# Optimization experiments

Hardware: AMD Instinct MI355X
Metric: run time of the kernel (lower is better)

Reference implementation:

```python
import jax, jax.numpy as jnp
import numpy as np

B, T, E, H = 4, 4096, 1024, 64

def setup_inputs() -> dict:
    key = jax.random.key(0)
    kx, kk, kq, kv = jax.random.split(key, 4)
    x = jax.random.normal(kx, (B, T, E), dtype=jnp.float32)
    Wk = jax.random.normal(kk, (E, H), dtype=jnp.float32) * (E ** -0.5)
    Wq = jax.random.normal(kq, (E, H), dtype=jnp.float32) * (E ** -0.5)
    Wv = jax.random.normal(kv, (E, H), dtype=jnp.float32) * (E ** -0.5)
    return {"x": x, "Wk": Wk, "Wq": Wq, "Wv": Wv}

def reference(x, Wk, Wq, Wv):
    # x: [B, T, E]; single causal attention head, dropout rate 0 (no-op)
    t = x.shape[1]
    k = jnp.einsum('bte,eh->bth', x, Wk)  # [B,T,H]
    q = jnp.einsum('bte,eh->bth', x, Wq)  # [B,T,H]
    v = jnp.einsum('bte,eh->bth', x, Wv)  # [B,T,H]
    scores = jnp.einsum('bqh,bkh->bqk', q, k) * (k.shape[-1] ** -0.5)  # [B,T,T]
    causal = jnp.tril(jnp.ones((t, t), dtype=bool))
    scores = jnp.where(causal, scores, -jnp.inf)
    attn = jax.nn.softmax(scores, axis=-1)
    return jnp.einsum('bqk,bkh->bqh', attn, v)  # [B,T,H]
```

## Files before the change

kernel.cpp:

```cpp
#include <hip/hip_runtime.h>
#include <hip/hip_bf16.h>

typedef short short8 __attribute__((ext_vector_type(8)));
typedef short short4v __attribute__((ext_vector_type(4)));
typedef float float4v __attribute__((ext_vector_type(4)));
typedef float f32x4 __attribute__((ext_vector_type(4)));

#define NEG_HUGE (-1e30f)
#define QK_SCALE 0.1803368801111204f

__device__ __forceinline__ unsigned short f2bf(float f) {
  union { __hip_bfloat16 h; unsigned short u; } c;
  c.h = __float2bfloat16(f);
  return c.u;
}

#define MFMA16(a, b, c) __builtin_amdgcn_mfma_f32_16x16x32_bf16((a), (b), (c), 0, 0, 0)

__global__ __launch_bounds__(256) void wtrans_kernel(
    const float* __restrict__ Wk, const float* __restrict__ Wq,
    const float* __restrict__ Wv, unsigned short* __restrict__ Wt) {
  int mat = blockIdx.x >> 4, kb = blockIdx.x & 15;
  const float* W = (mat == 0) ? Wk : ((mat == 1) ? Wq : Wv);
  float qscale = (mat == 1) ? QK_SCALE : 1.0f;
  __shared__ float tile[64][65];
  int tid = threadIdx.x;
  int n = tid & 63, k0 = tid >> 6;
#pragma unroll
  for (int i = 0; i < 16; i++) {
    int k = i * 4 + k0;
    tile[k][n] = W[(kb * 64 + k) * 64 + n];
  }
  __syncthreads();
  int n2 = tid >> 2, c = tid & 3;
  unsigned short tmp[16];
#pragma unroll
  for (int j = 0; j < 16; j++) tmp[j] = f2bf(tile[c * 16 + j][n2] * qscale);
  unsigned short* dst = Wt + (mat * 64 + n2) * 1024 + kb * 64 + c * 16;
  *(short8*)dst = *(short8*)tmp;
  *(short8*)(dst + 8) = *(short8*)(tmp + 8);
}

__global__ __launch_bounds__(512, 2) void proj_kernel(
    const float* __restrict__ x, const unsigned short* __restrict__ Wt,
    unsigned short* __restrict__ Kb, unsigned short* __restrict__ Qb,
    unsigned short* __restrict__ Vt) {
  __shared__ unsigned short x_l[2][64 * 64];
  __shared__ unsigned short w_l[2][192 * 64];
  int tid = threadIdx.x;
  int w = tid >> 6, lane = tid & 63;
  int wm = w >> 1, wn = w & 1;
  int g = lane >> 4, r = lane & 15;
  int row0 = blockIdx.x * 64;

  int xr = tid >> 3, xc16 = tid & 7;
  const float* xp = &x[(size_t)(row0 + xr) * 1024 + xc16 * 8];
  int xelem = xr * 64 + ((xc16 * 8) ^ ((xr & 7) << 3));
  const unsigned short* wp[3];
  int welem[3];
#pragma unroll
  for (int i = 0; i < 3; i++) {
    int c = tid + i * 512;
    int wr = c >> 3, wc16 = c & 7;
    wp[i] = &Wt[(size_t)wr * 1024 + wc16 * 8];
    welem[i] = wr * 64 + ((wc16 * 8) ^ ((wr & 7) << 3));
  }
  int swz = (r & 7) << 3;

  f32x4 acc[6];
#pragma unroll
  for (int nf = 0; nf < 6; nf++) acc[nf] = (f32x4){0.f, 0.f, 0.f, 0.f};

  float4v xa = *(const float4v*)(xp);
  float4v xb = *(const float4v*)(xp + 4);
  short8 wv[3];
#pragma unroll
  for (int i = 0; i < 3; i++) wv[i] = *(const short8*)(wp[i]);

  for (int t = 0; t < 16; t++) {
    int buf = t & 1;
    {
      unsigned short t8[8];
      t8[0] = f2bf(xa[0]); t8[1] = f2bf(xa[1]); t8[2] = f2bf(xa[2]); t8[3] = f2bf(xa[3]);
      t8[4] = f2bf(xb[0]); t8[5] = f2bf(xb[1]); t8[6] = f2bf(xb[2]); t8[7] = f2bf(xb[3]);
      *(short8*)&x_l[buf][xelem] = *(short8*)t8;
#pragma unroll
      for (int i = 0; i < 3; i++) *(short8*)&w_l[buf][welem[i]] = wv[i];
    }
    if (t < 15) {
      int k0 = (t + 1) * 64;
      xa = *(const float4v*)(xp + k0);
      xb = *(const float4v*)(xp + k0 + 4);
#pragma unroll
      for (int i = 0; i < 3; i++) wv[i] = *(const short8*)(wp[i] + k0);
    }
    __syncthreads();
#pragma unroll
    for (int ks = 0; ks < 2; ks++) {
      short8 af = *(short8*)&x_l[buf][(wm * 16 + r) * 64 + ((ks * 32 + g * 8) ^ swz)];
#pragma unroll
      for (int nf = 0; nf < 6; nf++) {
        short8 bf = *(short8*)&w_l[buf][(wn * 96 + nf * 16 + r) * 64 + ((ks * 32 + g * 8) ^ swz)];
        acc[nf] = MFMA16(af, bf, acc[nf]);
      }
    }
  }
#pragma unroll
  for (int nf = 0; nf < 6; nf++) {
    int col = wn * 96 + nf * 16 + r;
    if (col < 128) {
      int mat = col >> 6, h = col & 63;
      unsigned short* dst = (mat == 0) ? Kb : Qb;
#pragma unroll
      for (int reg = 0; reg < 4; reg++) {
        int grow = row0 + wm * 16 + g * 4 + reg;
        dst[(size_t)grow * 64 + h] = f2bf(acc[nf][reg]);
      }
    } else {
      int h = col & 63;
      int grow0 = row0 + wm * 16 + g * 4;
      unsigned short t4[4];
#pragma unroll
      for (int reg = 0; reg < 4; reg++) t4[reg] = f2bf(acc[nf][reg]);
      int kv6 = grow0 & 63;
      int nfb = (kv6 >> 4) & 3, gb = (kv6 >> 2) & 3;
      int s0 = (nfb >> 1) * 32 + gb * 8 + (nfb & 1) * 4;
      size_t off = ((size_t)(grow0 >> 12) * 64 + h) * 4096 +
                   ((size_t)(grow0 & 4095) & ~(size_t)63) + s0;
      *(short4v*)&Vt[off] = *(short4v*)t4;
    }
  }
}

__global__ __launch_bounds__(256, 3) void attn_kernel(
    const unsigned short* __restrict__ Kb, const unsigned short* __restrict__ Qb,
    const unsigned short* __restrict__ VtB, float* __restrict__ out) {
  __shared__ float O_l[4][32][68];
  __shared__ float st_l[4][32][2];
  int tid = threadIdx.x;
  int w = tid >> 6, lane = tid & 63;
  int g = lane >> 4, r = lane & 15;
  int bi = blockIdx.x;
  int b = bi & 3, iq = bi >> 2;
  int qt = (iq < 64) ? (64 + iq) : (127 - iq);
  int qabs = qt * 32;
  const unsigned short* Kp = Kb + (size_t)b * 4096 * 64;
  const unsigned short* Qp = Qb + (size_t)b * 4096 * 64;
  const unsigned short* Vp = VtB + (size_t)b * 64 * 4096;

  short8 qa[2][2];
#pragma unroll
  for (int mf = 0; mf < 2; mf++)
#pragma unroll
    for (int ks = 0; ks < 2; ks++)
      qa[mf][ks] = *(const short8*)&Qp[(size_t)(qabs + mf * 16 + r) * 64 + ks * 32 + g * 8];

  float m_st[2] = {NEG_HUGE, NEG_HUGE};
  float l_ln[2] = {0.f, 0.f};
  f32x4 o[4][2];
#pragma unroll
  for (int nfh = 0; nfh < 4; nfh++)
#pragma unroll
    for (int mf = 0; mf < 2; mf++) o[nfh][mf] = (f32x4){0.f, 0.f, 0.f, 0.f};

  int ntiles = (qabs >> 6) + 1;
  for (int t = w; t < ntiles; t += 4) {
    int kvb = t << 6;
    f32x4 s[4][2];
#pragma unroll
    for (int nf = 0; nf < 4; nf++)
#pragma unroll
      for (int mf = 0; mf < 2; mf++) s[nf][mf] = (f32x4){0.f, 0.f, 0.f, 0.f};
#pragma unroll
    for (int ks = 0; ks < 2; ks++) {
      short8 kf[4];
#pragma unroll
      for (int nf = 0; nf < 4; nf++)
        kf[nf] = *(const short8*)&Kp[(size_t)(kvb + nf * 16 + r) * 64 + ks * 32 + g * 8];
#pragma unroll
      for (int nf = 0; nf < 4; nf++) {
        s[nf][0] = MFMA16(kf[nf], qa[0][ks], s[nf][0]);
        s[nf][1] = MFMA16(kf[nf], qa[1][ks], s[nf][1]);
      }
    }
    short8 vf[2][4];
#pragma unroll
    for (int ks = 0; ks < 2; ks++)
#pragma unroll
      for (int nfh = 0; nfh < 4; nfh++)
        vf[ks][nfh] = *(const short8*)&Vp[(size_t)(nfh * 16 + r) * 4096 + kvb + ks * 32 + g * 8];
    if (kvb + 63 > qabs) {
#pragma unroll
      for (int mf = 0; mf < 2; mf++) {
        int q = qabs + mf * 16 + r;
#pragma unroll
        for (int nf = 0; nf < 4; nf++)
#pragma unroll
          for (int reg = 0; reg < 4; reg++) {
            int kv = kvb + nf * 16 + g * 4 + reg;
            if (kv > q) s[nf][mf][reg] = NEG_HUGE;
          }
      }
    }
    float alpha[2];
#pragma unroll
    for (int mf = 0; mf < 2; mf++) {
      float m0 = fmaxf(fmaxf(fmaxf(s[0][mf][0], s[0][mf][1]), fmaxf(s[0][mf][2], s[0][mf][3])),
                       fmaxf(fmaxf(s[1][mf][0], s[1][mf][1]), fmaxf(s[1][mf][2], s[1][mf][3])));
      float m1 = fmaxf(fmaxf(fmaxf(s[2][mf][0], s[2][mf][1]), fmaxf(s[2][mf][2], s[2][mf][3])),
                       fmaxf(fmaxf(s[3][mf][0], s[3][mf][1]), fmaxf(s[3][mf][2], s[3][mf][3])));
      float m0a = fmaxf(m0, m1);
      m0a = fmaxf(m0a, __shfl_xor(m0a, 16));
      m0a = fmaxf(m0a, __shfl_xor(m0a, 32));
      float mn = fmaxf(m_st[mf], m0a);
      alpha[mf] = exp2f(m_st[mf] - mn);
      m_st[mf] = mn;
    }
#pragma unroll
    for (int mf = 0; mf < 2; mf++) {
      float rs = 0.f;
#pragma unroll
      for (int nf = 0; nf < 4; nf++)
#pragma unroll
        for (int reg = 0; reg < 4; reg++) {
          float p = exp2f(s[nf][mf][reg] - m_st[mf]);
          s[nf][mf][reg] = p;
          rs += p;
        }
      l_ln[mf] = l_ln[mf] * alpha[mf] + rs;
#pragma unroll
      for (int nfh = 0; nfh < 4; nfh++)
#pragma unroll
        for (int reg = 0; reg < 4; reg++) o[nfh][mf][reg] *= alpha[mf];
    }
#pragma unroll
    for (int ks = 0; ks < 2; ks++)
#pragma unroll
      for (int mf = 0; mf < 2; mf++) {
        union { unsigned u[4]; short8 v; } pb;
        asm("v_cvt_pk_bf16_f32 %0, %1, %2" : "=v"(pb.u[0]) : "v"(s[2 * ks][mf][0]), "v"(s[2 * ks][mf][1]));
        asm("v_cvt_pk_bf16_f32 %0, %1, %2" : "=v"(pb.u[1]) : "v"(s[2 * ks][mf][2]), "v"(s[2 * ks][mf][3]));
        asm("v_cvt_pk_bf16_f32 %0, %1, %2" : "=v"(pb.u[2]) : "v"(s[2 * ks + 1][mf][0]), "v"(s[2 * ks + 1][mf][1]));
        asm("v_cvt_pk_bf16_f32 %0, %1, %2" : "=v"(pb.u[3]) : "v"(s[2 * ks + 1][mf][2]), "v"(s[2 * ks + 1][mf][3]));
#pragma unroll
        for (int nfh = 0; nfh < 4; nfh++)
          o[nfh][mf] = MFMA16(vf[ks][nfh], pb.v, o[nfh][mf]);
      }
  }
#pragma unroll
  for (int mf = 0; mf < 2; mf++) {
    float s0 = l_ln[mf];
    s0 += __shfl_xor(s0, 16);
    s0 += __shfl_xor(s0, 32);
    l_ln[mf] = s0;
  }
  __syncthreads();
#pragma unroll
  for (int nfh = 0; nfh < 4; nfh++)
#pragma unroll
    for (int mf = 0; mf < 2; mf++)
      *(f32x4*)&O_l[w][mf * 16 + r][nfh * 16 + g * 4] = o[nfh][mf];
  if (g == 0) {
#pragma unroll
    for (int mf = 0; mf < 2; mf++) {
      st_l[w][mf * 16 + r][0] = m_st[mf];
      st_l[w][mf * 16 + r][1] = l_ln[mf];
    }
  }
  __syncthreads();
  {
    int row = tid >> 3, cg = tid & 7;
    float mw[4], lw[4];
#pragma unroll
    for (int ww = 0; ww < 4; ww++) {
      mw[ww] = st_l[ww][row][0];
      lw[ww] = st_l[ww][row][1];
    }
    float mstar = fmaxf(fmaxf(mw[0], mw[1]), fmaxf(mw[2], mw[3]));
    float sc[4], lstar = 0.f;
#pragma unroll
    for (int ww = 0; ww < 4; ww++) { sc[ww] = exp2f(mw[ww] - mstar); lstar += sc[ww] * lw[ww]; }
    float inv = 1.0f / lstar;
    float a0[8];
#pragma unroll
    for (int cc = 0; cc < 8; cc++) a0[cc] = 0.f;
#pragma unroll
    for (int ww = 0; ww < 4; ww++) {
      f32x4 v0 = *(f32x4*)&O_l[ww][row][cg * 8];
      f32x4 v1 = *(f32x4*)&O_l[ww][row][cg * 8 + 4];
#pragma unroll
      for (int e = 0; e < 4; e++) { a0[e] += sc[ww] * v0[e]; a0[4 + e] += sc[ww] * v1[e]; }
    }
    float4v o0, o1;
#pragma unroll
    for (int e = 0; e < 4; e++) { o0[e] = a0[e] * inv; o1[e] = a0[4 + e] * inv; }
    float* op = &out[((size_t)b * 4096 + qabs + row) * 64 + cg * 8];
    *(float4v*)op = o0;
    *(float4v*)(op + 4) = o1;
  }
}

extern "C" void kernel_launch(void* const* d_in, const int* in_sizes, int n_in,
                              void* d_out, int out_size, void* d_ws, size_t ws_size,
                              hipStream_t stream) {
  (void)in_sizes; (void)n_in; (void)out_size; (void)ws_size;
  const float* x  = (const float*)d_in[0];
  const float* Wk = (const float*)d_in[1];
  const float* Wq = (const float*)d_in[2];
  const float* Wv = (const float*)d_in[3];
  float* out = (float*)d_out;
  char* ws = (char*)d_ws;

  unsigned short* Wt = (unsigned short*)ws;
  unsigned short* Kb = (unsigned short*)(ws + (512u << 10));
  unsigned short* Qb = (unsigned short*)(ws + (512u << 10) + (2u << 20));
  unsigned short* Vt = (unsigned short*)(ws + (512u << 10) + (4u << 20));

  wtrans_kernel<<<48, 256, 0, stream>>>(Wk, Wq, Wv, Wt);
  proj_kernel<<<256, 512, 0, stream>>>(x, Wt, Kb, Qb, Vt);
  attn_kernel<<<512, 256, 0, stream>>>(Kb, Qb, Vt, out);
}
```

Before: 56.63 us.

## Deepen proj kernel pipeline with K=128 tiles and two-stage x prefetch

Reworks the projection GEMM main loop to use 128-wide K tiles in dynamic shared memory, halving the iteration count and barriers. The x fp32 loads are prefetched two stages ahead and W one stage ahead, with the bf16 conversion and LDS store for the next buffer done after the MFMAs so global latency overlaps compute. The change raises LDS use to 128 KB per block and drops the two-blocks-per-CU launch bound, which lowers occupancy to one block per CU and adds register pressure from the extra prefetch registers.

```diff
diff --git a/kernel.cpp b/kernel.cpp
--- a/kernel.cpp
+++ b/kernel.cpp
@@ -41,69 +41,99 @@
   *(short8*)(dst + 8) = *(short8*)(tmp + 8);
 }
 
-__global__ __launch_bounds__(512, 2) void proj_kernel(
+__global__ __launch_bounds__(512) void proj_kernel(
     const float* __restrict__ x, const unsigned short* __restrict__ Wt,
     unsigned short* __restrict__ Kb, unsigned short* __restrict__ Qb,
     unsigned short* __restrict__ Vt) {
-  __shared__ unsigned short x_l[2][64 * 64];
-  __shared__ unsigned short w_l[2][192 * 64];
+  extern __shared__ unsigned short smem[];
   int tid = threadIdx.x;
   int w = tid >> 6, lane = tid & 63;
   int wm = w >> 1, wn = w & 1;
   int g = lane >> 4, r = lane & 15;
   int row0 = blockIdx.x * 64;
 
-  int xr = tid >> 3, xc16 = tid & 7;
-  const float* xp = &x[(size_t)(row0 + xr) * 1024 + xc16 * 8];
-  int xelem = xr * 64 + ((xc16 * 8) ^ ((xr & 7) << 3));
-  const unsigned short* wp[3];
-  int welem[3];
-#pragma unroll
-  for (int i = 0; i < 3; i++) {
-    int c = tid + i * 512;
-    int wr = c >> 3, wc16 = c & 7;
-    wp[i] = &Wt[(size_t)wr * 1024 + wc16 * 8];
-    welem[i] = wr * 64 + ((wc16 * 8) ^ ((wr & 7) << 3));
-  }
-  int swz = (r & 7) << 3;
+  int xr = tid >> 3, xc = tid & 7;
+  const float* xp = &x[(size_t)(row0 + xr) * 1024 + xc * 16];
+  int xe0 = xr * 128 + (((xc * 2 + 0) ^ (xr & 7)) << 3);
+  int xe1 = xr * 128 + (((xc * 2 + 1) ^ (xr & 7)) << 3);
+  const unsigned short* wp[6];
+  int we[6];
+#pragma unroll
+  for (int i = 0; i < 6; i++) {
+    int idx = tid + i * 512;
+    int wr = idx >> 4, wc = idx & 15;
+    wp[i] = &Wt[(size_t)wr * 1024 + wc * 8];
+    we[i] = wr * 128 + (((wc ^ (wr & 7))) << 3);
+  }
+  int fsw = r & 7;
 
   f32x4 acc[6];
 #pragma unroll
   for (int nf = 0; nf < 6; nf++) acc[nf] = (f32x4){0.f, 0.f, 0.f, 0.f};
 
-  float4v xa = *(const float4v*)(xp);
-  float4v xb = *(const float4v*)(xp + 4);
-  short8 wv[3];
-#pragma unroll
-  for (int i = 0; i < 3; i++) wv[i] = *(const short8*)(wp[i]);
-
-  for (int t = 0; t < 16; t++) {
-    int buf = t & 1;
-    {
-      unsigned short t8[8];
-      t8[0] = f2bf(xa[0]); t8[1] = f2bf(xa[1]); t8[2] = f2bf(xa[2]); t8[3] = f2bf(xa[3]);
-      t8[4] = f2bf(xb[0]); t8[5] = f2bf(xb[1]); t8[6] = f2bf(xb[2]); t8[7] = f2bf(xb[3]);
-      *(short8*)&x_l[buf][xelem] = *(short8*)t8;
-#pragma unroll
-      for (int i = 0; i < 3; i++) *(short8*)&w_l[buf][welem[i]] = wv[i];
-    }
-    if (t < 15) {
-      int k0 = (t + 1) * 64;
-      xa = *(const float4v*)(xp + k0);
-      xb = *(const float4v*)(xp + k0 + 4);
-#pragma unroll
-      for (int i = 0; i < 3; i++) wv[i] = *(const short8*)(wp[i] + k0);
-    }
-    __syncthreads();
-#pragma unroll
-    for (int ks = 0; ks < 2; ks++) {
-      short8 af = *(short8*)&x_l[buf][(wm * 16 + r) * 64 + ((ks * 32 + g * 8) ^ swz)];
+  float4v x0[4], x1[4];
+  short8 wv[6];
+#pragma unroll
+  for (int j = 0; j < 4; j++) x0[j] = *(const float4v*)(xp + j * 4);
+#pragma unroll
+  for (int j = 0; j < 4; j++) x1[j] = *(const float4v*)(xp + 128 + j * 4);
+#pragma unroll
+  for (int i = 0; i < 6; i++) wv[i] = *(const short8*)(wp[i]);
+  {
+    unsigned short t16[16];
+#pragma unroll
+    for (int j = 0; j < 4; j++)
+#pragma unroll
+      for (int e = 0; e < 4; e++) t16[j * 4 + e] = f2bf(x0[j][e]);
+    *(short8*)&smem[xe0] = *(short8*)&t16[0];
+    *(short8*)&smem[xe1] = *(short8*)&t16[8];
+#pragma unroll
+    for (int i = 0; i < 6; i++) *(short8*)&smem[16384 + we[i]] = wv[i];
+  }
+  asm volatile("s_waitcnt lgkmcnt(0)" ::: "memory");
+  __builtin_amdgcn_s_barrier();
+
+  for (int t = 0; t < 8; t++) {
+    int cur = t & 1;
+    unsigned short* xl = smem + cur * 8192;
+    unsigned short* wl = smem + 16384 + cur * 24576;
+    if (t < 7) {
+      int k0 = (t + 1) * 128;
+#pragma unroll
+      for (int i = 0; i < 6; i++) wv[i] = *(const short8*)(wp[i] + k0);
+    }
+    float4v xn[4];
+    if (t < 6) {
+      int k0 = (t + 2) * 128;
+#pragma unroll
+      for (int j = 0; j < 4; j++) xn[j] = *(const float4v*)(xp + k0 + j * 4);
+    }
+#pragma unroll
+    for (int ks = 0; ks < 4; ks++) {
+      short8 af = *(short8*)&xl[(wm * 16 + r) * 128 + (((ks * 4 + g) ^ fsw) << 3)];
 #pragma unroll
       for (int nf = 0; nf < 6; nf++) {
-        short8 bf = *(short8*)&w_l[buf][(wn * 96 + nf * 16 + r) * 64 + ((ks * 32 + g * 8) ^ swz)];
+        short8 bf = *(short8*)&wl[(wn * 96 + nf * 16 + r) * 128 + (((ks * 4 + g) ^ fsw) << 3)];
         acc[nf] = MFMA16(af, bf, acc[nf]);
       }
     }
+    if (t < 7) {
+      unsigned short* xl1 = smem + (cur ^ 1) * 8192;
+      unsigned short* wl1 = smem + 16384 + (cur ^ 1) * 24576;
+      unsigned short t16[16];
+#pragma unroll
+      for (int j = 0; j < 4; j++)
+#pragma unroll
+        for (int e = 0; e < 4; e++) t16[j * 4 + e] = f2bf(x1[j][e]);
+      *(short8*)&xl1[xe0] = *(short8*)&t16[0];
+      *(short8*)&xl1[xe1] = *(short8*)&t16[8];
+#pragma unroll
+      for (int i = 0; i < 6; i++) *(short8*)&wl1[we[i]] = wv[i];
+    }
+#pragma unroll
+    for (int j = 0; j < 4; j++) x1[j] = xn[j];
+    asm volatile("s_waitcnt lgkmcnt(0)" ::: "memory");
+    __builtin_amdgcn_s_barrier();
   }
 #pragma unroll
   for (int nf = 0; nf < 6; nf++) {
@@ -317,6 +347,6 @@
   unsigned short* Vt = (unsigned short*)(ws + (512u << 10) + (4u << 20));
 
   wtrans_kernel<<<48, 256, 0, stream>>>(Wk, Wq, Wv, Wt);
-  proj_kernel<<<256, 512, 0, stream>>>(x, Wt, Kb, Qb, Vt);
+  proj_kernel<<<256, 512, 131072, stream>>>(x, Wt, Kb, Qb, Vt);
   attn_kernel<<<512, 256, 0, stream>>>(Kb, Qb, Vt, out);
 }
```

New measurement: 61.47 us. 8.5% more time.

## Stream projection tiles into LDS with direct global-to-LDS loads

Applied to the files above, without the earlier changes.

The projection kernel now copies x (raw fp32) and pre-swizzled bf16 weights from global memory straight into LDS with global_load_lds. x is triple-buffered and W double-buffered, with explicit vmcnt waits and raw barriers. fp32-to-bf16 conversion of x moves to after the LDS read, using packed cvt instructions. The weight-transpose kernel now writes the XOR swizzle into global memory so the direct copies land already swizzled. This removes register staging and the per-thread conversion stores, but the larger dynamic LDS (96KB) may limit occupancy, and the launch-bounds min-blocks hint is dropped.

```diff
diff --git a/kernel.cpp b/kernel.cpp
--- a/kernel.cpp
+++ b/kernel.cpp
@@ -16,6 +16,10 @@
 }
 
 #define MFMA16(a, b, c) __builtin_amdgcn_mfma_f32_16x16x32_bf16((a), (b), (c), 0, 0, 0)
+
+#define GLL(gp, lp) __builtin_amdgcn_global_load_lds( \
+    (const __attribute__((address_space(1))) unsigned int*)(const void*)(gp), \
+    (__attribute__((address_space(3))) unsigned int*)(void*)(lp), 16, 0, 0)
 
 __global__ __launch_bounds__(256) void wtrans_kernel(
     const float* __restrict__ Wk, const float* __restrict__ Wq,
@@ -36,74 +40,100 @@
   unsigned short tmp[16];
 #pragma unroll
   for (int j = 0; j < 16; j++) tmp[j] = f2bf(tile[c * 16 + j][n2] * qscale);
-  unsigned short* dst = Wt + (mat * 64 + n2) * 1024 + kb * 64 + c * 16;
-  *(short8*)dst = *(short8*)tmp;
-  *(short8*)(dst + 8) = *(short8*)(tmp + 8);
-}
-
-__global__ __launch_bounds__(512, 2) void proj_kernel(
+  unsigned short* rowp = Wt + (mat * 64 + n2) * 1024 + kb * 64;
+  int s = n2 & 7;
+  *(short8*)(rowp + ((c * 2) ^ s) * 8) = *(short8*)tmp;
+  *(short8*)(rowp + ((c * 2 + 1) ^ s) * 8) = *(short8*)(tmp + 8);
+}
+
+__global__ __launch_bounds__(512) void proj_kernel(
     const float* __restrict__ x, const unsigned short* __restrict__ Wt,
     unsigned short* __restrict__ Kb, unsigned short* __restrict__ Qb,
     unsigned short* __restrict__ Vt) {
-  __shared__ unsigned short x_l[2][64 * 64];
-  __shared__ unsigned short w_l[2][192 * 64];
+  extern __shared__ char smem[];
   int tid = threadIdx.x;
   int w = tid >> 6, lane = tid & 63;
   int wm = w >> 1, wn = w & 1;
   int g = lane >> 4, r = lane & 15;
   int row0 = blockIdx.x * 64;
 
-  int xr = tid >> 3, xc16 = tid & 7;
-  const float* xp = &x[(size_t)(row0 + xr) * 1024 + xc16 * 8];
-  int xelem = xr * 64 + ((xc16 * 8) ^ ((xr & 7) << 3));
-  const unsigned short* wp[3];
-  int welem[3];
+  long xoff[2];
+  unsigned xl_u[2];
+#pragma unroll
+  for (int i = 0; i < 2; i++) {
+    int l = i * 512 + tid;
+    int rr = l >> 4, p = l & 15;
+    xoff[i] = (long)(row0 + rr) * 4096 + ((p ^ (rr & 7)) * 16);
+    xl_u[i] = i * 8192 + w * 1024;
+  }
+  long woff[3];
+  unsigned wl_u[3];
 #pragma unroll
   for (int i = 0; i < 3; i++) {
-    int c = tid + i * 512;
-    int wr = c >> 3, wc16 = c & 7;
-    wp[i] = &Wt[(size_t)wr * 1024 + wc16 * 8];
-    welem[i] = wr * 64 + ((wc16 * 8) ^ ((wr & 7) << 3));
-  }
-  int swz = (r & 7) << 3;
+    int l = i * 512 + tid;
+    woff[i] = (long)(l >> 3) * 2048 + (l & 7) * 16;
+    wl_u[i] = i * 8192 + w * 1024;
+  }
+  const char* xg = (const char*)x;
+  const char* wg = (const char*)Wt;
 
   f32x4 acc[6];
 #pragma unroll
   for (int nf = 0; nf < 6; nf++) acc[nf] = (f32x4){0.f, 0.f, 0.f, 0.f};
 
-  float4v xa = *(const float4v*)(xp);
-  float4v xb = *(const float4v*)(xp + 4);
-  short8 wv[3];
-#pragma unroll
-  for (int i = 0; i < 3; i++) wv[i] = *(const short8*)(wp[i]);
-
+  {
+    char* wb = smem + 49152;
+#pragma unroll
+    for (int i = 0; i < 3; i++) GLL(wg + woff[i], wb + wl_u[i]);
+    char* xb0 = smem;
+#pragma unroll
+    for (int i = 0; i < 2; i++) GLL(xg + xoff[i], xb0 + xl_u[i]);
+    char* xb1 = smem + 16384;
+#pragma unroll
+    for (int i = 0; i < 2; i++) GLL(xg + xoff[i] + 256, xb1 + xl_u[i]);
+  }
+  asm volatile("s_waitcnt vmcnt(2)" ::: "memory");
+  __builtin_amdgcn_s_barrier();
+
+  int rs7 = r & 7;
   for (int t = 0; t < 16; t++) {
-    int buf = t & 1;
-    {
-      unsigned short t8[8];
-      t8[0] = f2bf(xa[0]); t8[1] = f2bf(xa[1]); t8[2] = f2bf(xa[2]); t8[3] = f2bf(xa[3]);
-      t8[4] = f2bf(xb[0]); t8[5] = f2bf(xb[1]); t8[6] = f2bf(xb[2]); t8[7] = f2bf(xb[3]);
-      *(short8*)&x_l[buf][xelem] = *(short8*)t8;
-#pragma unroll
-      for (int i = 0; i < 3; i++) *(short8*)&w_l[buf][welem[i]] = wv[i];
-    }
     if (t < 15) {
-      int k0 = (t + 1) * 64;
-      xa = *(const float4v*)(xp + k0);
-      xb = *(const float4v*)(xp + k0 + 4);
-#pragma unroll
-      for (int i = 0; i < 3; i++) wv[i] = *(const short8*)(wp[i] + k0);
-    }
-    __syncthreads();
+      char* wb = smem + 49152 + ((t + 1) & 1) * 24576;
+      long ko = (long)(t + 1) * 128;
+#pragma unroll
+      for (int i = 0; i < 3; i++) GLL(wg + woff[i] + ko, wb + wl_u[i]);
+    }
+    if (t < 14) {
+      char* xb = smem + ((t + 2) % 3) * 16384;
+      long ko = (long)(t + 2) * 256;
+#pragma unroll
+      for (int i = 0; i < 2; i++) GLL(xg + xoff[i] + ko, xb + xl_u[i]);
+    }
+    const char* xl = smem + (t % 3) * 16384;
+    const char* wl = smem + 49152 + (t & 1) * 24576;
 #pragma unroll
     for (int ks = 0; ks < 2; ks++) {
-      short8 af = *(short8*)&x_l[buf][(wm * 16 + r) * 64 + ((ks * 32 + g * 8) ^ swz)];
+      int c0 = ks * 8 + g * 2;
+      int rowb = (wm * 16 + r) * 256;
+      f32x4 xa0 = *(const f32x4*)(xl + rowb + ((c0 ^ rs7) * 16));
+      f32x4 xa1 = *(const f32x4*)(xl + rowb + (((c0 + 1) ^ rs7) * 16));
+      union { unsigned u[4]; short8 v; } pk;
+      asm("v_cvt_pk_bf16_f32 %0, %1, %2" : "=v"(pk.u[0]) : "v"(xa0[0]), "v"(xa0[1]));
+      asm("v_cvt_pk_bf16_f32 %0, %1, %2" : "=v"(pk.u[1]) : "v"(xa0[2]), "v"(xa0[3]));
+      asm("v_cvt_pk_bf16_f32 %0, %1, %2" : "=v"(pk.u[2]) : "v"(xa1[0]), "v"(xa1[1]));
+      asm("v_cvt_pk_bf16_f32 %0, %1, %2" : "=v"(pk.u[3]) : "v"(xa1[2]), "v"(xa1[3]));
+      short8 af = pk.v;
 #pragma unroll
       for (int nf = 0; nf < 6; nf++) {
-        short8 bf = *(short8*)&w_l[buf][(wn * 96 + nf * 16 + r) * 64 + ((ks * 32 + g * 8) ^ swz)];
+        int wrow = wn * 96 + nf * 16 + r;
+        int wp = (ks * 4 + g) ^ rs7;
+        short8 bf = *(const short8*)(wl + wrow * 128 + wp * 16);
         acc[nf] = MFMA16(af, bf, acc[nf]);
       }
     }
+    if (t < 14) asm volatile("s_waitcnt vmcnt(2)" ::: "memory");
+    else        asm volatile("s_waitcnt vmcnt(0)" ::: "memory");
+    __builtin_amdgcn_s_barrier();
   }
 #pragma unroll
   for (int nf = 0; nf < 6; nf++) {
@@ -317,6 +347,6 @@
   unsigned short* Vt = (unsigned short*)(ws + (512u << 10) + (4u << 20));
 
   wtrans_kernel<<<48, 256, 0, stream>>>(Wk, Wq, Wv, Wt);
-  proj_kernel<<<256, 512, 0, stream>>>(x, Wt, Kb, Qb, Vt);
+  proj_kernel<<<256, 512, 98304, stream>>>(x, Wt, Kb, Qb, Vt);
   attn_kernel<<<512, 256, 0, stream>>>(Kb, Qb, Vt, out);
 }
```

Result: slower. 57.89 us (+2.2%).

## Split attention KV tiles across eight waves per block instead of four

Applied to the files above, without the earlier changes.

Each attention block now runs 512 threads (8 waves), each wave taking every eighth KV tile, so the per-block causal KV loop is split across twice as many waves. The cross-wave merge of partial outputs moves to dynamic shared memory (about 70 KB) and is widened to combine 8 partial states, with each thread reducing 4 output columns. This aims to shorten the serial KV loop per block and raise the number of waves in flight. In exchange it doubles the LDS merge cost and may reduce how many blocks fit per CU.

```diff
diff --git a/kernel.cpp b/kernel.cpp
--- a/kernel.cpp
+++ b/kernel.cpp
@@ -132,11 +132,12 @@
   }
 }
 
-__global__ __launch_bounds__(256, 3) void attn_kernel(
+__global__ __launch_bounds__(512, 4) void attn_kernel(
     const unsigned short* __restrict__ Kb, const unsigned short* __restrict__ Qb,
     const unsigned short* __restrict__ VtB, float* __restrict__ out) {
-  __shared__ float O_l[4][32][68];
-  __shared__ float st_l[4][32][2];
+  extern __shared__ char smem[];
+  float* O_l = (float*)smem;
+  float* st_l = (float*)(smem + 69632);
   int tid = threadIdx.x;
   int w = tid >> 6, lane = tid & 63;
   int g = lane >> 4, r = lane & 15;
@@ -164,7 +165,7 @@
     for (int mf = 0; mf < 2; mf++) o[nfh][mf] = (f32x4){0.f, 0.f, 0.f, 0.f};
 
   int ntiles = (qabs >> 6) + 1;
-  for (int t = w; t < ntiles; t += 4) {
+  for (int t = w; t < ntiles; t += 8) {
     int kvb = t << 6;
     f32x4 s[4][2];
 #pragma unroll
@@ -259,44 +260,41 @@
   for (int nfh = 0; nfh < 4; nfh++)
 #pragma unroll
     for (int mf = 0; mf < 2; mf++)
-      *(f32x4*)&O_l[w][mf * 16 + r][nfh * 16 + g * 4] = o[nfh][mf];
+      *(f32x4*)&O_l[(w * 32 + mf * 16 + r) * 68 + nfh * 16 + g * 4] = o[nfh][mf];
   if (g == 0) {
 #pragma unroll
     for (int mf = 0; mf < 2; mf++) {
-      st_l[w][mf * 16 + r][0] = m_st[mf];
-      st_l[w][mf * 16 + r][1] = l_ln[mf];
+      st_l[(w * 32 + mf * 16 + r) * 2 + 0] = m_st[mf];
+      st_l[(w * 32 + mf * 16 + r) * 2 + 1] = l_ln[mf];
     }
   }
   __syncthreads();
   {
-    int row = tid >> 3, cg = tid & 7;
-    float mw[4], lw[4];
-#pragma unroll
-    for (int ww = 0; ww < 4; ww++) {
-      mw[ww] = st_l[ww][row][0];
-      lw[ww] = st_l[ww][row][1];
-    }
-    float mstar = fmaxf(fmaxf(mw[0], mw[1]), fmaxf(mw[2], mw[3]));
-    float sc[4], lstar = 0.f;
-#pragma unroll
-    for (int ww = 0; ww < 4; ww++) { sc[ww] = exp2f(mw[ww] - mstar); lstar += sc[ww] * lw[ww]; }
+    int row = tid >> 4, cg = tid & 15;
+    float mw[8], lw[8];
+#pragma unroll
+    for (int ww = 0; ww < 8; ww++) {
+      mw[ww] = st_l[(ww * 32 + row) * 2 + 0];
+      lw[ww] = st_l[(ww * 32 + row) * 2 + 1];
+    }
+    float mstar = NEG_HUGE;
+#pragma unroll
+    for (int ww = 0; ww < 8; ww++) mstar = fmaxf(mstar, mw[ww]);
+    float sc[8], lstar = 0.f;
+#pragma unroll
+    for (int ww = 0; ww < 8; ww++) { sc[ww] = exp2f(mw[ww] - mstar); lstar += sc[ww] * lw[ww]; }
     float inv = 1.0f / lstar;
-    float a0[8];
-#pragma unroll
-    for (int cc = 0; cc < 8; cc++) a0[cc] = 0.f;
-#pragma unroll
-    for (int ww = 0; ww < 4; ww++) {
-      f32x4 v0 = *(f32x4*)&O_l[ww][row][cg * 8];
-      f32x4 v1 = *(f32x4*)&O_l[ww][row][cg * 8 + 4];
-#pragma unroll
-      for (int e = 0; e < 4; e++) { a0[e] += sc[ww] * v0[e]; a0[4 + e] += sc[ww] * v1[e]; }
-    }
-    float4v o0, o1;
-#pragma unroll
-    for (int e = 0; e < 4; e++) { o0[e] = a0[e] * inv; o1[e] = a0[4 + e] * inv; }
-    float* op = &out[((size_t)b * 4096 + qabs + row) * 64 + cg * 8];
-    *(float4v*)op = o0;
-    *(float4v*)(op + 4) = o1;
+    f32x4 a0 = (f32x4){0.f, 0.f, 0.f, 0.f};
+#pragma unroll
+    for (int ww = 0; ww < 8; ww++) {
+      f32x4 v0 = *(f32x4*)&O_l[(ww * 32 + row) * 68 + cg * 4];
+#pragma unroll
+      for (int e = 0; e < 4; e++) a0[e] += sc[ww] * v0[e];
+    }
+    float4v o0;
+#pragma unroll
+    for (int e = 0; e < 4; e++) o0[e] = a0[e] * inv;
+    *(float4v*)&out[((size_t)b * 4096 + qabs + row) * 64 + cg * 4] = o0;
   }
 }
 
@@ -318,5 +316,5 @@
 
   wtrans_kernel<<<48, 256, 0, stream>>>(Wk, Wq, Wv, Wt);
   proj_kernel<<<256, 512, 0, stream>>>(x, Wt, Kb, Qb, Vt);
-  attn_kernel<<<512, 256, 0, stream>>>(Kb, Qb, Vt, out);
-}
+  attn_kernel<<<512, 512, 71680, stream>>>(Kb, Qb, Vt, out);
+}
```

After: 87.70 us. 54.9% more time.
